# Performance work log

Measured on AMD Instinct MI355X. Metric: run time of the kernel, lower is better.

The kernel has to match this reference:

```python
import jax, jax.numpy as jnp
import numpy as np

N = 50000      # nodes
E = 400000     # edges
F_NODE = 16    # node_features
F_EDGE = 8     # edge_features
H = 16         # hidden_dim
HID_MLP = 32   # edge-MLP hidden width (from MLP([edge_features, 32, ...]))
G = 64         # graphs in batch
T = 2          # num_targets
EPS = 1e-5


def setup_inputs() -> dict:
    key = jax.random.key(0)
    ks = jax.random.split(key, 16)
    def nrm(k, shape, s=0.05):
        return jax.random.normal(k, shape, jnp.float32) * s
    z = lambda *s: jnp.zeros(s, jnp.float32)
    o = lambda *s: jnp.ones(s, jnp.float32)
    inp = {}
    inp['x'] = jax.random.normal(ks[0], (N, F_NODE), jnp.float32)
    inp['edge_attr'] = jax.random.normal(ks[1], (E, F_EDGE), jnp.float32)
    # conv1 edge-MLP: Linear(F_EDGE,32) -> BN -> ReLU -> Linear(32, F_NODE*H)
    inp['e1_W1'] = nrm(ks[2], (F_EDGE, HID_MLP)); inp['e1_b1'] = z(HID_MLP)
    inp['e1_g'] = o(HID_MLP); inp['e1_be'] = z(HID_MLP)
    inp['e1_W2'] = nrm(ks[3], (HID_MLP, F_NODE * H)); inp['e1_b2'] = z(F_NODE * H)
    inp['c1_root'] = nrm(ks[4], (F_NODE, H)); inp['c1_bias'] = z(H)
    # conv2 edge-MLP: Linear(F_EDGE,32) -> BN -> ReLU -> Linear(32, H*H)
    inp['e2_W1'] = nrm(ks[5], (F_EDGE, HID_MLP)); inp['e2_b1'] = z(HID_MLP)
    inp['e2_g'] = o(HID_MLP); inp['e2_be'] = z(HID_MLP)
    inp['e2_W2'] = nrm(ks[6], (HID_MLP, H * H)); inp['e2_b2'] = z(H * H)
    inp['c2_root'] = nrm(ks[7], (H, H)); inp['c2_bias'] = z(H)
    # node batch norms
    inp['bn1_g'] = o(H); inp['bn1_b'] = z(H)
    inp['bn2_g'] = o(H); inp['bn2_b'] = z(H)
    # head MLP
    inp['fc1_W'] = nrm(ks[8], (H, H)); inp['fc1_b'] = z(H)
    inp['fc2_W'] = nrm(ks[9], (H, T)); inp['fc2_b'] = z(T)
    # int args
    inp['edge_index'] = jax.random.randint(ks[10], (2, E), 0, N, dtype=jnp.int32).astype(jnp.int64)
    inp['batch'] = jnp.sort(jax.random.randint(ks[11], (N,), 0, G, dtype=jnp.int32)).astype(jnp.int64)
    return inp


def _bn(h, g, b):
    # training-mode BatchNorm1d: batch stats, biased variance
    m = h.mean(0)
    v = jnp.mean((h - m) ** 2, axis=0)
    return g * (h - m) / jnp.sqrt(v + EPS) + b


def _edge_mlp(e, W1, b1, g, be, W2, b2):
    h = jax.nn.relu(_bn(e @ W1 + b1, g, be))
    return h @ W2 + b2


def _seg_mean(vals, idx, num):
    s = jax.ops.segment_sum(vals, idx, num_segments=num)
    c = jax.ops.segment_sum(jnp.ones((idx.shape[0],), vals.dtype), idx, num_segments=num)
    return s / jnp.maximum(c, 1.0)[:, None]


def _nnconv(x, src, dst, e, W1, b1, g, be, W2, b2, Wroot, bias, in_c, out_c):
    w = _edge_mlp(e, W1, b1, g, be, W2, b2).reshape(-1, in_c, out_c)  # [E, in, out]
    msg = jnp.einsum('ei,eio->eo', x[src], w)                        # gather + per-edge matmul
    agg = _seg_mean(msg, dst, x.shape[0])                            # scatter-mean into targets
    return agg + x @ Wroot + bias


def reference(x, edge_attr, e1_W1, e1_b1, e1_g, e1_be, e1_W2, e1_b2, c1_root, c1_bias,
              e2_W1, e2_b1, e2_g, e2_be, e2_W2, e2_b2, c2_root, c2_bias,
              bn1_g, bn1_b, bn2_g, bn2_b, fc1_W, fc1_b, fc2_W, fc2_b,
              edge_index, batch):
    src, dst = edge_index[0], edge_index[1]
    h = _nnconv(x, src, dst, edge_attr, e1_W1, e1_b1, e1_g, e1_be, e1_W2, e1_b2,
                c1_root, c1_bias, F_NODE, H)
    h = jax.nn.relu(_bn(h, bn1_g, bn1_b))
    h = _nnconv(h, src, dst, edge_attr, e2_W1, e2_b1, e2_g, e2_be, e2_W2, e2_b2,
                c2_root, c2_bias, H, H)
    h = jax.nn.relu(_bn(h, bn2_g, bn2_b))
    pooled = _seg_mean(h, batch, G)          # global_mean_pool -> [G, H]
    out = jax.nn.relu(pooled @ fc1_W + fc1_b) @ fc2_W + fc2_b
    return out
```

## Files before the change

kernel.cpp:

```cpp
#include <hip/hip_runtime.h>

#define N_NODES 50000
#define N_EDGES 400000
#define NG 64
#define NT 2
#define EPS 1e-5f
#define NB_N ((N_NODES + 255) / 256)
#define NB_E ((N_EDGES + 255) / 256)
#define NB_A ((N_NODES + 31) / 32)

constexpr int mom_i(int t) {
    int tt = t - 8; int i = 0;
    while (tt >= 8 - i) { tt -= 8 - i; ++i; }
    return i;
}
constexpr int mom_j(int t) {
    int tt = t - 8; int i = 0;
    while (tt >= 8 - i) { tt -= 8 - i; ++i; }
    return i + tt;
}

template<int IDX>
__device__ __forceinline__ float mom_term(const float* v) {
    if constexpr (IDX >= 44) return 0.f;
    else if constexpr (IDX < 8) return v[IDX];
    else return v[mom_i(IDX)] * v[mom_j(IDX)];
}

template<int BASE>
__device__ __forceinline__ void mom_add16(const float* v, float* acc) {
    acc[0]  += mom_term<BASE + 0>(v);
    acc[1]  += mom_term<BASE + 1>(v);
    acc[2]  += mom_term<BASE + 2>(v);
    acc[3]  += mom_term<BASE + 3>(v);
    acc[4]  += mom_term<BASE + 4>(v);
    acc[5]  += mom_term<BASE + 5>(v);
    acc[6]  += mom_term<BASE + 6>(v);
    acc[7]  += mom_term<BASE + 7>(v);
    acc[8]  += mom_term<BASE + 8>(v);
    acc[9]  += mom_term<BASE + 9>(v);
    acc[10] += mom_term<BASE + 10>(v);
    acc[11] += mom_term<BASE + 11>(v);
    acc[12] += mom_term<BASE + 12>(v);
    acc[13] += mom_term<BASE + 13>(v);
    acc[14] += mom_term<BASE + 14>(v);
    acc[15] += mom_term<BASE + 15>(v);
}

template<int BASE>
__device__ __forceinline__ void mom_loop(
    const float* __restrict__ ea, const int* __restrict__ dst,
    int* __restrict__ deg, float* acc)
{
    const int stride = gridDim.x * 256;
    for (int e = blockIdx.x * 256 + threadIdx.x; e < N_EDGES; e += stride) {
        const float4 a4 = ((const float4*)ea)[e * 2];
        const float4 b4 = ((const float4*)ea)[e * 2 + 1];
        const float v[8] = {a4.x,a4.y,a4.z,a4.w, b4.x,b4.y,b4.z,b4.w};
        if constexpr (BASE == 0) atomicAdd(deg + dst[e], 1);
        mom_add16<BASE>(v, acc);
    }
}

__global__ __launch_bounds__(256) void k_moments(
    const float* __restrict__ ea, const int* __restrict__ dst,
    float* __restrict__ mom, int* __restrict__ deg)
{
    const int c = blockIdx.y;
    float acc[16];
    #pragma unroll
    for (int u = 0; u < 16; ++u) acc[u] = 0.f;
    switch (c) {
        case 0: mom_loop<0 >(ea, dst, deg, acc); break;
        case 1: mom_loop<16>(ea, dst, deg, acc); break;
        default: mom_loop<32>(ea, dst, deg, acc); break;
    }
    __shared__ float red[4][16];
    const int lane = threadIdx.x & 63, wv = threadIdx.x >> 6;
    #pragma unroll
    for (int u = 0; u < 16; ++u) {
        float s = acc[u];
        #pragma unroll
        for (int o = 32; o; o >>= 1) s += __shfl_down(s, o);
        if (lane == 0) red[wv][u] = s;
    }
    __syncthreads();
    if (threadIdx.x < 16) {
        const int idx = c * 16 + threadIdx.x;
        if (idx < 44) {
            const float s = red[0][threadIdx.x] + red[1][threadIdx.x]
                          + red[2][threadIdx.x] + red[3][threadIdx.x];
            atomicAdd(mom + idx, s);
        }
    }
}

__global__ __launch_bounds__(256) void k_scan1(
    const int* __restrict__ deg, int* __restrict__ loc, int* __restrict__ bsum,
    int* __restrict__ hist)
{
    __shared__ int s[256];
    __shared__ int shist[128];
    const int t = threadIdx.x;
    const int n = blockIdx.x * 256 + t;
    const int v = (n < N_NODES) ? deg[n] : 0;
    if (t < 128) shist[t] = 0;
    s[t] = v;
    __syncthreads();
    #pragma unroll
    for (int d = 1; d < 256; d <<= 1) {
        const int a = (t >= d) ? s[t - d] : 0;
        __syncthreads();
        s[t] += a;
        __syncthreads();
    }
    if (n < N_NODES) {
        loc[n] = s[t] - v;
        atomicAdd(&shist[min(v, 127)], 1);
    }
    if (t == 255) bsum[blockIdx.x] = s[t];
    __syncthreads();
    if (t < 128 && shist[t]) atomicAdd(hist + t, shist[t]);
}

__global__ __launch_bounds__(256) void k_singles(
    int* __restrict__ bsum, const float* __restrict__ mom,
    const float* __restrict__ W1a, const float* __restrict__ b1a,
    const float* __restrict__ ga,  const float* __restrict__ bea,
    const float* __restrict__ W1b, const float* __restrict__ b1b,
    const float* __restrict__ gb,  const float* __restrict__ beb,
    float* __restrict__ ss, const int* __restrict__ batch,
    int* __restrict__ start, const int* __restrict__ hist,
    int* __restrict__ cursor)
{
    __shared__ int s[256];
    const int t = threadIdx.x;
    const int v = (t < NB_N) ? bsum[t] : 0;
    s[t] = v;
    __syncthreads();
    #pragma unroll
    for (int d = 1; d < 256; d <<= 1) {
        const int a = (t >= d) ? s[t - d] : 0;
        __syncthreads();
        s[t] += a;
        __syncthreads();
    }
    if (t < NB_N) bsum[t] = s[t] - v;

    if (t < 64) {
        const int m = t >> 5, k = t & 31;
        const float* W1 = m ? W1b : W1a;
        const float b   = (m ? b1b : b1a)[k];
        const float g   = (m ? gb  : ga)[k];
        const float be  = (m ? beb : bea)[k];
        float w[8];
        #pragma unroll
        for (int j = 0; j < 8; ++j) w[j] = W1[j * 32 + k];
        float Sw = 0.f;
        #pragma unroll
        for (int j = 0; j < 8; ++j) Sw += mom[j] * w[j];
        float q = 0.f;
        int idx = 8;
        #pragma unroll
        for (int i = 0; i < 8; ++i)
            #pragma unroll
            for (int j = i; j < 8; ++j) {
                const float Mv = mom[idx++];
                q += Mv * w[i] * w[j] * (i == j ? 1.f : 2.f);
            }
        const float invE  = 1.0f / (float)N_EDGES;
        const float sump  = Sw + (float)N_EDGES * b;
        const float sumpp = q + 2.f * b * Sw + (float)N_EDGES * b * b;
        const float mean  = sump * invE;
        const float var   = fmaxf(sumpp * invE - mean * mean, 0.f);
        const float sc    = g * rsqrtf(var + EPS);
        ss[m * 64 + k]      = sc;
        ss[m * 64 + 32 + k] = be - mean * sc;
    }
    if (t <= NG) {
        int lo = 0, hi = N_NODES;
        while (lo < hi) {
            const int mid = (lo + hi) >> 1;
            if (batch[mid] < t) lo = mid + 1; else hi = mid;
        }
        start[t] = lo;
    }
    if (t == 0) {
        int acc = 0;
        for (int d = 127; d >= 0; --d) { cursor[d] = acc; acc += hist[d]; }
    }
}

__global__ __launch_bounds__(256) void k_scan3(
    const int* __restrict__ loc, const int* __restrict__ bsum,
    const int* __restrict__ deg, int* __restrict__ off, int* __restrict__ cur,
    int* __restrict__ cursor, int* __restrict__ perm)
{
    __shared__ int scnt[128];
    __shared__ int sbase[128];
    const int t = threadIdx.x;
    const int n = blockIdx.x * 256 + t;
    if (t < 128) scnt[t] = 0;
    __syncthreads();
    int b = 0, rk = 0;
    if (n < N_NODES) {
        const int o = loc[n] + bsum[n >> 8];
        off[n] = o; cur[n] = o;
        if (n == 0) off[N_NODES] = N_EDGES;
        b  = min(deg[n], 127);
        rk = atomicAdd(&scnt[b], 1);
    }
    __syncthreads();
    if (t < 128 && scnt[t]) sbase[t] = atomicAdd(cursor + t, scnt[t]);
    __syncthreads();
    if (n < N_NODES) perm[sbase[b] + rk] = n;
}

__global__ __launch_bounds__(256) void k_pos(
    const int* __restrict__ src, const int* __restrict__ dst,
    const float* __restrict__ ea, int* __restrict__ cur,
    int* __restrict__ src_s, float4* __restrict__ ea_s)
{
    const int e = blockIdx.x * 256 + threadIdx.x;
    if (e < N_EDGES) {
        const float4 a4 = ((const float4*)ea)[e * 2];
        const float4 b4 = ((const float4*)ea)[e * 2 + 1];
        const int p = atomicAdd(cur + dst[e], 1);
        src_s[p] = src[e];
        ea_s[p * 2]     = a4;
        ea_s[p * 2 + 1] = b4;
    }
}

__global__ __launch_bounds__(256) void k_agg(
    const float* __restrict__ x, const float4* __restrict__ ea_s,
    const int* __restrict__ src_s, const int* __restrict__ off,
    const int* __restrict__ perm,
    const float* __restrict__ W1, const float* __restrict__ W2,
    const float* __restrict__ ss,
    float* __restrict__ agg_out, float* __restrict__ xsum_out)
{
    __shared__ float4 sW2q[2048];
    const int tid = threadIdx.x;
    #pragma unroll
    for (int i = 0; i < 8; ++i) {
        const int f = tid + 256 * i;
        sW2q[f ^ ((f >> 8) & 7)] = ((const float4*)W2)[f];
    }
    __syncthreads();

    const int c  = tid & 7;
    const int g  = blockIdx.x * 32 + (tid >> 3);
    if (g >= N_NODES) return;
    const int n  = perm[g];

    float w1r[32];
    #pragma unroll
    for (int j = 0; j < 8; ++j)
        #pragma unroll
        for (int kk = 0; kk < 4; ++kk)
            w1r[j * 4 + kk] = W1[j * 32 + c * 4 + kk];
    float scr[4], shr[4];
    #pragma unroll
    for (int kk = 0; kk < 4; ++kk) {
        scr[kk] = ss[c * 4 + kk];
        shr[kk] = ss[32 + c * 4 + kk];
    }

    const int o0 = off[n], o1 = off[n + 1];
    const int len = o1 - o0;
    float T[64];
    #pragma unroll
    for (int j = 0; j < 64; ++j) T[j] = 0.f;
    float xs0 = 0.f, xs1 = 0.f;

    float4 ca, cb, cx0, cx1, cx2, cx3;
    float4 pa, pb;
    int    snn = 0;
    if (len > 0) {
        const int s0 = src_s[o0];
        ca = ea_s[(size_t)o0 * 2];
        cb = ea_s[(size_t)o0 * 2 + 1];
        const float4* xp = (const float4*)(x + (size_t)s0 * 16);
        cx0 = xp[0]; cx1 = xp[1]; cx2 = xp[2]; cx3 = xp[3];
        pa = ca; pb = cb;
        if (len > 1) {
            snn = src_s[o0 + 1];
            pa = ea_s[(size_t)(o0 + 1) * 2];
            pb = ea_s[(size_t)(o0 + 1) * 2 + 1];
        }
    }
    for (int r = 0; r < len; ++r) {
        float4 nx0 = cx0, nx1 = cx1, nx2 = cx2, nx3 = cx3;
        float4 qa = pa, qb = pb;
        int sn2 = snn;
        if (r + 1 < len) {
            const float4* xp = (const float4*)(x + (size_t)snn * 16);
            nx0 = xp[0]; nx1 = xp[1]; nx2 = xp[2]; nx3 = xp[3];
        }
        if (r + 2 < len) {
            sn2 = src_s[o0 + r + 2];
            qa = ea_s[(size_t)(o0 + r + 2) * 2];
            qb = ea_s[(size_t)(o0 + r + 2) * 2 + 1];
        }
        const float ein[8] = {ca.x,ca.y,ca.z,ca.w, cb.x,cb.y,cb.z,cb.w};
        float h[4];
        #pragma unroll
        for (int kk = 0; kk < 4; ++kk) {
            float p = 0.f;
            #pragma unroll
            for (int j = 0; j < 8; ++j) p += ein[j] * w1r[j * 4 + kk];
            h[kk] = fmaxf(p * scr[kk] + shr[kk], 0.f);
        }
        const float xv[16] = {cx0.x,cx0.y,cx0.z,cx0.w, cx1.x,cx1.y,cx1.z,cx1.w,
                              cx2.x,cx2.y,cx2.z,cx2.w, cx3.x,cx3.y,cx3.z,cx3.w};
        #pragma unroll
        for (int kk = 0; kk < 4; ++kk) {
            const float hk = h[kk];
            #pragma unroll
            for (int i = 0; i < 16; ++i) T[kk * 16 + i] += hk * xv[i];
        }
        xs0 += xv[c * 2];
        xs1 += xv[c * 2 + 1];
        ca = pa; cb = pb;
        cx0 = nx0; cx1 = nx1; cx2 = nx2; cx3 = nx3;
        pa = qa; pb = qb; snn = sn2;
    }

    float agg[16];
    #pragma unroll
    for (int o = 0; o < 16; ++o) agg[o] = 0.f;
    #pragma unroll
    for (int kk = 0; kk < 4; ++kk) {
        const int fbase = (c * 4 + kk) * 64;
        #pragma unroll
        for (int i = 0; i < 16; ++i) {
            const float tv = T[kk * 16 + i];
            const int f0 = fbase + i * 4;
            const float4 w0 = sW2q[(f0 + 0) ^ c];
            const float4 w1 = sW2q[(f0 + 1) ^ c];
            const float4 w2 = sW2q[(f0 + 2) ^ c];
            const float4 w3 = sW2q[(f0 + 3) ^ c];
            agg[0]+=tv*w0.x; agg[1]+=tv*w0.y; agg[2]+=tv*w0.z; agg[3]+=tv*w0.w;
            agg[4]+=tv*w1.x; agg[5]+=tv*w1.y; agg[6]+=tv*w1.z; agg[7]+=tv*w1.w;
            agg[8]+=tv*w2.x; agg[9]+=tv*w2.y; agg[10]+=tv*w2.z; agg[11]+=tv*w2.w;
            agg[12]+=tv*w3.x; agg[13]+=tv*w3.y; agg[14]+=tv*w3.z; agg[15]+=tv*w3.w;
        }
    }
    #pragma unroll
    for (int m = 1; m < 8; m <<= 1) {
        #pragma unroll
        for (int o = 0; o < 16; ++o) agg[o] += __shfl_xor(agg[o], m);
    }
    ((float2*)(agg_out  + (size_t)n * 16))[c] = make_float2(agg[c * 2], agg[c * 2 + 1]);
    ((float2*)(xsum_out + (size_t)n * 16))[c] = make_float2(xs0, xs1);
}

__global__ __launch_bounds__(256) void k_node_pre(
    const float* __restrict__ agg, const float* __restrict__ xsum,
    const int* __restrict__ off, const float* __restrict__ xin,
    const float* __restrict__ root, const float* __restrict__ b2,
    const float* __restrict__ bias, float* __restrict__ bnstats,
    float* __restrict__ pre_out)
{
    __shared__ float sroot[256], sb2[256], sbias[16], lacc[32];
    const int tid = threadIdx.x;
    if (tid < 64) {
        ((float4*)sroot)[tid] = ((const float4*)root)[tid];
        ((float4*)sb2)[tid]   = ((const float4*)b2)[tid];
    }
    if (tid < 16) sbias[tid] = bias[tid];
    if (tid < 32) lacc[tid] = 0.f;
    __syncthreads();

    const int n = blockIdx.x * 256 + tid;
    const bool valid = (n < N_NODES);
    float pre[16];
    if (valid) {
        float acc[16];
        const float4* ap = (const float4*)(agg + (size_t)n * 16);
        const float4 a0 = ap[0], a1 = ap[1], a2 = ap[2], a3 = ap[3];
        acc[0]=a0.x; acc[1]=a0.y; acc[2]=a0.z; acc[3]=a0.w;
        acc[4]=a1.x; acc[5]=a1.y; acc[6]=a1.z; acc[7]=a1.w;
        acc[8]=a2.x; acc[9]=a2.y; acc[10]=a2.z; acc[11]=a2.w;
        acc[12]=a3.x; acc[13]=a3.y; acc[14]=a3.z; acc[15]=a3.w;
        const float4* sp = (const float4*)(xsum + (size_t)n * 16);
        const float4 s0 = sp[0], s1 = sp[1], s2 = sp[2], s3 = sp[3];
        const float sv[16] = {s0.x,s0.y,s0.z,s0.w, s1.x,s1.y,s1.z,s1.w,
                              s2.x,s2.y,s2.z,s2.w, s3.x,s3.y,s3.z,s3.w};
        #pragma unroll
        for (int i = 0; i < 16; ++i) {
            const float si = sv[i];
            #pragma unroll
            for (int o = 0; o < 16; ++o) acc[o] += si * sb2[i * 16 + o];
        }
        const float inv = 1.0f / (float)max(off[n + 1] - off[n], 1);
        const float4* xp = (const float4*)(xin + (size_t)n * 16);
        const float4 x0=xp[0],x1=xp[1],x2=xp[2],x3=xp[3];
        const float xn[16] = {x0.x,x0.y,x0.z,x0.w, x1.x,x1.y,x1.z,x1.w,
                              x2.x,x2.y,x2.z,x2.w, x3.x,x3.y,x3.z,x3.w};
        #pragma unroll
        for (int o = 0; o < 16; ++o) pre[o] = sbias[o] + acc[o] * inv;
        #pragma unroll
        for (int i = 0; i < 16; ++i) {
            const float xi = xn[i];
            #pragma unroll
            for (int o = 0; o < 16; ++o) pre[o] += xi * sroot[i * 16 + o];
        }
        float4* wp4 = (float4*)(pre_out + (size_t)n * 16);
        wp4[0] = make_float4(pre[0],pre[1],pre[2],pre[3]);
        wp4[1] = make_float4(pre[4],pre[5],pre[6],pre[7]);
        wp4[2] = make_float4(pre[8],pre[9],pre[10],pre[11]);
        wp4[3] = make_float4(pre[12],pre[13],pre[14],pre[15]);
    } else {
        #pragma unroll
        for (int o = 0; o < 16; ++o) pre[o] = 0.f;
    }
    const int lane = tid & 63;
    #pragma unroll
    for (int o = 0; o < 16; ++o) {
        float s = pre[o], q = s * s;
        #pragma unroll
        for (int w = 32; w; w >>= 1) {
            s += __shfl_down(s, w);
            q += __shfl_down(q, w);
        }
        if (lane == 0) { atomicAdd(&lacc[o], s); atomicAdd(&lacc[16 + o], q); }
    }
    __syncthreads();
    if (tid < 32) atomicAdd(bnstats + tid, lacc[tid]);
}

__global__ __launch_bounds__(256) void k_node_bn(
    const float* __restrict__ pre, const float* __restrict__ bnstats,
    const float* __restrict__ gam, const float* __restrict__ bet,
    float* __restrict__ hout)
{
    __shared__ float sscale[16], sshift[16];
    const int tid = threadIdx.x;
    if (tid < 16) {
        const float mean = bnstats[tid] * (1.0f / N_NODES);
        const float var  = fmaxf(bnstats[16 + tid] * (1.0f / N_NODES) - mean * mean, 0.f);
        const float rs   = rsqrtf(var + EPS);
        const float sc   = gam[tid] * rs;
        sscale[tid] = sc;
        sshift[tid] = bet[tid] - mean * sc;
    }
    __syncthreads();
    const int n = blockIdx.x * 256 + tid;
    if (n >= N_NODES) return;
    const float4* pp = (const float4*)(pre + (size_t)n * 16);
    const float4 p0=pp[0],p1=pp[1],p2=pp[2],p3=pp[3];
    const float pv[16] = {p0.x,p0.y,p0.z,p0.w, p1.x,p1.y,p1.z,p1.w,
                          p2.x,p2.y,p2.z,p2.w, p3.x,p3.y,p3.z,p3.w};
    float h[16];
    #pragma unroll
    for (int o = 0; o < 16; ++o) h[o] = fmaxf(pv[o] * sscale[o] + sshift[o], 0.f);
    float4* hp = (float4*)(hout + (size_t)n * 16);
    hp[0] = make_float4(h[0],h[1],h[2],h[3]);
    hp[1] = make_float4(h[4],h[5],h[6],h[7]);
    hp[2] = make_float4(h[8],h[9],h[10],h[11]);
    hp[3] = make_float4(h[12],h[13],h[14],h[15]);
}

__global__ __launch_bounds__(256) void k_pool_bn(
    const float* __restrict__ pre, const float* __restrict__ bnstats,
    const float* __restrict__ gam, const float* __restrict__ bet,
    const int* __restrict__ start, float* __restrict__ pool)
{
    __shared__ float lds[16][16];
    __shared__ float sscale[16], sshift[16];
    const int tid = threadIdx.x;
    if (tid < 16) {
        const float mean = bnstats[tid] * (1.0f / N_NODES);
        const float var  = fmaxf(bnstats[16 + tid] * (1.0f / N_NODES) - mean * mean, 0.f);
        const float rs   = rsqrtf(var + EPS);
        const float sc   = gam[tid] * rs;
        sscale[tid] = sc;
        sshift[tid] = bet[tid] - mean * sc;
    }
    __syncthreads();
    const int g = blockIdx.x;
    const int c = tid & 15, rg = tid >> 4;
    const int s = start[g], e = start[g + 1];
    const float sc = sscale[c], sh = sshift[c];
    float acc = 0.f;
    for (int r = s + rg; r < e; r += 16)
        acc += fmaxf(pre[(size_t)r * 16 + c] * sc + sh, 0.f);
    lds[rg][c] = acc;
    __syncthreads();
    if (tid < 16) {
        float sum = 0.f;
        #pragma unroll
        for (int i = 0; i < 16; ++i) sum += lds[i][tid];
        const float inv = 1.0f / (float)max(e - s, 1);
        pool[g * 16 + tid] = sum * inv;
    }
}

__global__ __launch_bounds__(64) void k_head(
    const float* __restrict__ pool,
    const float* __restrict__ fc1W, const float* __restrict__ fc1b,
    const float* __restrict__ fc2W, const float* __restrict__ fc2b,
    float* __restrict__ out)
{
    const int g = threadIdx.x;
    if (g >= NG) return;
    float p[16];
    #pragma unroll
    for (int o = 0; o < 16; ++o) p[o] = pool[g * 16 + o];
    float z[16];
    #pragma unroll
    for (int j = 0; j < 16; ++j) {
        float a = fc1b[j];
        #pragma unroll
        for (int o = 0; o < 16; ++o) a += p[o] * fc1W[o * 16 + j];
        z[j] = fmaxf(a, 0.f);
    }
    #pragma unroll
    for (int t = 0; t < NT; ++t) {
        float a = fc2b[t];
        #pragma unroll
        for (int j = 0; j < 16; ++j) a += z[j] * fc2W[j * 2 + t];
        out[g * 2 + t] = a;
    }
}

extern "C" void kernel_launch(void* const* d_in, const int* in_sizes, int n_in,
                              void* d_out, int out_size, void* d_ws, size_t ws_size,
                              hipStream_t stream)
{
    const float* x    = (const float*)d_in[0];
    const float* ea   = (const float*)d_in[1];
    const float* e1W1 = (const float*)d_in[2];  const float* e1b1 = (const float*)d_in[3];
    const float* e1g  = (const float*)d_in[4];  const float* e1be = (const float*)d_in[5];
    const float* e1W2 = (const float*)d_in[6];  const float* e1b2 = (const float*)d_in[7];
    const float* c1r  = (const float*)d_in[8];  const float* c1b  = (const float*)d_in[9];
    const float* e2W1 = (const float*)d_in[10]; const float* e2b1 = (const float*)d_in[11];
    const float* e2g  = (const float*)d_in[12]; const float* e2be = (const float*)d_in[13];
    const float* e2W2 = (const float*)d_in[14]; const float* e2b2 = (const float*)d_in[15];
    const float* c2r  = (const float*)d_in[16]; const float* c2b  = (const float*)d_in[17];
    const float* bn1g = (const float*)d_in[18]; const float* bn1b = (const float*)d_in[19];
    const float* bn2g = (const float*)d_in[20]; const float* bn2b = (const float*)d_in[21];
    const float* fc1W = (const float*)d_in[22]; const float* fc1b = (const float*)d_in[23];
    const float* fc2W = (const float*)d_in[24]; const float* fc2b = (const float*)d_in[25];
    const int* eidx   = (const int*)d_in[26];
    const int* batch  = (const int*)d_in[27];
    const int* src = eidx;
    const int* dst = eidx + N_EDGES;

    float* ws      = (float*)d_ws;
    float* mom     = ws;
    float* bnstats = ws + 64;
    float* ss      = ws + 128;
    int* hist_i    = (int*)(ws + 256);
    int* cursor_i  = (int*)(ws + 384);
    int* deg_i   = (int*)(ws + 512);
    int* loc_i   = deg_i + N_NODES;
    int* cur_i   = loc_i + N_NODES;
    int* bsum_i  = cur_i + N_NODES;
    int* start_i = bsum_i + 256;
    int* off_i   = start_i + 72;
    int* perm_i  = off_i + N_NODES + 8;
    int* src_s   = perm_i + N_NODES;
    const size_t fo = 512 + 256 + 72 + 8 + 5 * (size_t)N_NODES + (size_t)N_EDGES;
    float* ea_s  = ws + fo;
    float* aggb  = ea_s + (size_t)N_EDGES * 8;
    float* xsumb = aggb + (size_t)N_NODES * 16;
    float* pre1  = xsumb + (size_t)N_NODES * 16;
    float* h1n   = pre1 + (size_t)N_NODES * 16;
    float* pool  = h1n + (size_t)N_NODES * 16;

    hipMemsetAsync(d_ws, 0, (size_t)(512 + N_NODES) * sizeof(float), stream);

    k_moments<<<dim3(512, 3), 256, 0, stream>>>(ea, dst, mom, deg_i);
    k_scan1<<<NB_N, 256, 0, stream>>>(deg_i, loc_i, bsum_i, hist_i);
    k_singles<<<1, 256, 0, stream>>>(bsum_i, mom, e1W1, e1b1, e1g, e1be,
                                     e2W1, e2b1, e2g, e2be, ss, batch, start_i,
                                     hist_i, cursor_i);
    k_scan3<<<NB_N, 256, 0, stream>>>(loc_i, bsum_i, deg_i, off_i, cur_i,
                                      cursor_i, perm_i);
    k_pos<<<NB_E, 256, 0, stream>>>(src, dst, ea, cur_i, src_s, (float4*)ea_s);

    k_agg<<<NB_A, 256, 0, stream>>>(x, (const float4*)ea_s, src_s, off_i, perm_i,
                                    e1W1, e1W2, ss, aggb, xsumb);
    k_node_pre<<<NB_N, 256, 0, stream>>>(aggb, xsumb, off_i, x, c1r, e1b2,
                                         c1b, bnstats, pre1);
    k_node_bn<<<NB_N, 256, 0, stream>>>(pre1, bnstats, bn1g, bn1b, h1n);

    k_agg<<<NB_A, 256, 0, stream>>>(h1n, (const float4*)ea_s, src_s, off_i, perm_i,
                                    e2W1, e2W2, ss + 64, aggb, xsumb);
    k_node_pre<<<NB_N, 256, 0, stream>>>(aggb, xsumb, off_i, h1n, c2r, e2b2,
                                         c2b, bnstats + 32, pre1);

    k_pool_bn<<<NG, 256, 0, stream>>>(pre1, bnstats + 32, bn2g, bn2b, start_i, pool);
    k_head<<<1, 64, 0, stream>>>(pool, fc1W, fc1b, fc2W, fc2b, (float*)d_out);
}
```

Baseline: 237.0 us.

## Fuse moment passes into one sweep and simplify k_agg prefetch and projection indexing

k_moments now computes all 44 edge-attribute moments in a single pass over the edges with 48 accumulators per thread on a 1-D grid of 192 blocks. Previously it ran three grid slices that each re-read edge_attr. In k_agg the prefetch loop drops its bounds checks: src_s and ea_s are padded with a few dummy entries so reads past the segment stay safe. The per-thread xsum values now come from a direct float2 load, the loop is unrolled by two, and the W2 projection uses precomputed base pointers with a simpler XOR swizzle. The changes are meant to cut redundant global reads and branch and index overhead, at the cost of more registers, possibly lower occupancy, and workspace layout shifts that must stay consistent.

```diff
diff --git a/kernel.cpp b/kernel.cpp
--- a/kernel.cpp
+++ b/kernel.cpp
@@ -47,51 +47,37 @@
     acc[15] += mom_term<BASE + 15>(v);
 }
 
-template<int BASE>
-__device__ __forceinline__ void mom_loop(
+__global__ __launch_bounds__(256) void k_moments(
     const float* __restrict__ ea, const int* __restrict__ dst,
-    int* __restrict__ deg, float* acc)
-{
+    float* __restrict__ mom, int* __restrict__ deg)
+{
+    float acc[48];
+    #pragma unroll
+    for (int u = 0; u < 48; ++u) acc[u] = 0.f;
     const int stride = gridDim.x * 256;
     for (int e = blockIdx.x * 256 + threadIdx.x; e < N_EDGES; e += stride) {
         const float4 a4 = ((const float4*)ea)[e * 2];
         const float4 b4 = ((const float4*)ea)[e * 2 + 1];
         const float v[8] = {a4.x,a4.y,a4.z,a4.w, b4.x,b4.y,b4.z,b4.w};
-        if constexpr (BASE == 0) atomicAdd(deg + dst[e], 1);
-        mom_add16<BASE>(v, acc);
-    }
-}
-
-__global__ __launch_bounds__(256) void k_moments(
-    const float* __restrict__ ea, const int* __restrict__ dst,
-    float* __restrict__ mom, int* __restrict__ deg)
-{
-    const int c = blockIdx.y;
-    float acc[16];
-    #pragma unroll
-    for (int u = 0; u < 16; ++u) acc[u] = 0.f;
-    switch (c) {
-        case 0: mom_loop<0 >(ea, dst, deg, acc); break;
-        case 1: mom_loop<16>(ea, dst, deg, acc); break;
-        default: mom_loop<32>(ea, dst, deg, acc); break;
-    }
-    __shared__ float red[4][16];
+        atomicAdd(deg + dst[e], 1);
+        mom_add16<0 >(v, acc);
+        mom_add16<16>(v, acc + 16);
+        mom_add16<32>(v, acc + 32);
+    }
+    __shared__ float red[4][48];
     const int lane = threadIdx.x & 63, wv = threadIdx.x >> 6;
     #pragma unroll
-    for (int u = 0; u < 16; ++u) {
+    for (int u = 0; u < 48; ++u) {
         float s = acc[u];
         #pragma unroll
         for (int o = 32; o; o >>= 1) s += __shfl_down(s, o);
         if (lane == 0) red[wv][u] = s;
     }
     __syncthreads();
-    if (threadIdx.x < 16) {
-        const int idx = c * 16 + threadIdx.x;
-        if (idx < 44) {
-            const float s = red[0][threadIdx.x] + red[1][threadIdx.x]
-                          + red[2][threadIdx.x] + red[3][threadIdx.x];
-            atomicAdd(mom + idx, s);
-        }
+    if (threadIdx.x < 44) {
+        const float s = red[0][threadIdx.x] + red[1][threadIdx.x]
+                      + red[2][threadIdx.x] + red[3][threadIdx.x];
+        atomicAdd(mom + threadIdx.x, s);
     }
 }
 
@@ -229,8 +215,27 @@
         src_s[p] = src[e];
         ea_s[p * 2]     = a4;
         ea_s[p * 2 + 1] = b4;
-    }
-}
+        if (e < 4) src_s[N_EDGES + e] = 0;
+    }
+}
+
+#define PROJ(IX)                                                              \
+    _Pragma("unroll")                                                         \
+    for (int kk = 0; kk < 4; ++kk) {                                          \
+        _Pragma("unroll")                                                     \
+        for (int i = 0; i < 16; ++i) {                                        \
+            const float tv = T[kk * 16 + i];                                  \
+            const int fo4 = kk * 64 + ((i ^ IX) << 2);                        \
+            const float4 w0 = pk0[fo4];                                       \
+            const float4 w1 = pk1[fo4];                                       \
+            const float4 w2 = pk2[fo4];                                       \
+            const float4 w3 = pk3[fo4];                                       \
+            agg[0]+=tv*w0.x; agg[1]+=tv*w0.y; agg[2]+=tv*w0.z; agg[3]+=tv*w0.w;\
+            agg[4]+=tv*w1.x; agg[5]+=tv*w1.y; agg[6]+=tv*w1.z; agg[7]+=tv*w1.w;\
+            agg[8]+=tv*w2.x; agg[9]+=tv*w2.y; agg[10]+=tv*w2.z; agg[11]+=tv*w2.w;\
+            agg[12]+=tv*w3.x; agg[13]+=tv*w3.y; agg[14]+=tv*w3.z; agg[15]+=tv*w3.w;\
+        }                                                                     \
+    }
 
 __global__ __launch_bounds__(256) void k_agg(
     const float* __restrict__ x, const float4* __restrict__ ea_s,
@@ -274,35 +279,32 @@
     for (int j = 0; j < 64; ++j) T[j] = 0.f;
     float xs0 = 0.f, xs1 = 0.f;
 
-    float4 ca, cb, cx0, cx1, cx2, cx3;
-    float4 pa, pb;
+    float4 ca = make_float4(0,0,0,0), cb = ca;
+    float4 cx0 = ca, cx1 = ca, cx2 = ca, cx3 = ca;
+    float2 cxs = make_float2(0, 0);
+    float4 pa = ca, pb = ca;
     int    snn = 0;
+    const int* sp2 = src_s + o0 + 2;
+    const float4* ep2 = ea_s + (size_t)(o0 + 2) * 2;
     if (len > 0) {
         const int s0 = src_s[o0];
         ca = ea_s[(size_t)o0 * 2];
         cb = ea_s[(size_t)o0 * 2 + 1];
-        const float4* xp = (const float4*)(x + (size_t)s0 * 16);
+        const float4* xp = (const float4*)(x + (s0 << 4));
         cx0 = xp[0]; cx1 = xp[1]; cx2 = xp[2]; cx3 = xp[3];
-        pa = ca; pb = cb;
-        if (len > 1) {
-            snn = src_s[o0 + 1];
-            pa = ea_s[(size_t)(o0 + 1) * 2];
-            pb = ea_s[(size_t)(o0 + 1) * 2 + 1];
-        }
-    }
+        cxs = *(const float2*)(x + (s0 << 4) + (c << 1));
+        snn = src_s[o0 + 1];
+        pa = ea_s[(size_t)(o0 + 1) * 2];
+        pb = ea_s[(size_t)(o0 + 1) * 2 + 1];
+    }
+    #pragma unroll 2
     for (int r = 0; r < len; ++r) {
-        float4 nx0 = cx0, nx1 = cx1, nx2 = cx2, nx3 = cx3;
-        float4 qa = pa, qb = pb;
-        int sn2 = snn;
-        if (r + 1 < len) {
-            const float4* xp = (const float4*)(x + (size_t)snn * 16);
-            nx0 = xp[0]; nx1 = xp[1]; nx2 = xp[2]; nx3 = xp[3];
-        }
-        if (r + 2 < len) {
-            sn2 = src_s[o0 + r + 2];
-            qa = ea_s[(size_t)(o0 + r + 2) * 2];
-            qb = ea_s[(size_t)(o0 + r + 2) * 2 + 1];
-        }
+        const float4* xp = (const float4*)(x + (snn << 4));
+        const float4 nx0 = xp[0], nx1 = xp[1], nx2 = xp[2], nx3 = xp[3];
+        const float2 nxs = *(const float2*)(x + (snn << 4) + (c << 1));
+        const int sn2 = sp2[r];
+        const float4 qa = ep2[(size_t)r * 2];
+        const float4 qb = ep2[(size_t)r * 2 + 1];
         const float ein[8] = {ca.x,ca.y,ca.z,ca.w, cb.x,cb.y,cb.z,cb.w};
         float h[4];
         #pragma unroll
@@ -320,33 +322,24 @@
             #pragma unroll
             for (int i = 0; i < 16; ++i) T[kk * 16 + i] += hk * xv[i];
         }
-        xs0 += xv[c * 2];
-        xs1 += xv[c * 2 + 1];
-        ca = pa; cb = pb;
+        xs0 += cxs.x;
+        xs1 += cxs.y;
+        ca = pa; cb = pb; pa = qa; pb = qb;
         cx0 = nx0; cx1 = nx1; cx2 = nx2; cx3 = nx3;
-        pa = qa; pb = qb; snn = sn2;
-    }
-
+        cxs = nxs; snn = sn2;
+    }
+
+    const int cA = c & 3;
+    const int iX = (c >> 2) & 1;
+    const float4* pk0 = sW2q + (c << 8) + (0 ^ cA);
+    const float4* pk1 = sW2q + (c << 8) + (1 ^ cA);
+    const float4* pk2 = sW2q + (c << 8) + (2 ^ cA);
+    const float4* pk3 = sW2q + (c << 8) + (3 ^ cA);
     float agg[16];
     #pragma unroll
     for (int o = 0; o < 16; ++o) agg[o] = 0.f;
-    #pragma unroll
-    for (int kk = 0; kk < 4; ++kk) {
-        const int fbase = (c * 4 + kk) * 64;
-        #pragma unroll
-        for (int i = 0; i < 16; ++i) {
-            const float tv = T[kk * 16 + i];
-            const int f0 = fbase + i * 4;
-            const float4 w0 = sW2q[(f0 + 0) ^ c];
-            const float4 w1 = sW2q[(f0 + 1) ^ c];
-            const float4 w2 = sW2q[(f0 + 2) ^ c];
-            const float4 w3 = sW2q[(f0 + 3) ^ c];
-            agg[0]+=tv*w0.x; agg[1]+=tv*w0.y; agg[2]+=tv*w0.z; agg[3]+=tv*w0.w;
-            agg[4]+=tv*w1.x; agg[5]+=tv*w1.y; agg[6]+=tv*w1.z; agg[7]+=tv*w1.w;
-            agg[8]+=tv*w2.x; agg[9]+=tv*w2.y; agg[10]+=tv*w2.z; agg[11]+=tv*w2.w;
-            agg[12]+=tv*w3.x; agg[13]+=tv*w3.y; agg[14]+=tv*w3.z; agg[15]+=tv*w3.w;
-        }
-    }
+    if (iX == 0) { PROJ(0) } else { PROJ(1) }
+
     #pragma unroll
     for (int m = 1; m < 8; m <<= 1) {
         #pragma unroll
@@ -563,9 +556,9 @@
     int* off_i   = start_i + 72;
     int* perm_i  = off_i + N_NODES + 8;
     int* src_s   = perm_i + N_NODES;
-    const size_t fo = 512 + 256 + 72 + 8 + 5 * (size_t)N_NODES + (size_t)N_EDGES;
+    const size_t fo = 512 + 256 + 72 + 8 + 5 * (size_t)N_NODES + (size_t)N_EDGES + 8;
     float* ea_s  = ws + fo;
-    float* aggb  = ea_s + (size_t)N_EDGES * 8;
+    float* aggb  = ea_s + (size_t)(N_EDGES + 4) * 8;
     float* xsumb = aggb + (size_t)N_NODES * 16;
     float* pre1  = xsumb + (size_t)N_NODES * 16;
     float* h1n   = pre1 + (size_t)N_NODES * 16;
@@ -573,7 +566,7 @@
 
     hipMemsetAsync(d_ws, 0, (size_t)(512 + N_NODES) * sizeof(float), stream);
 
-    k_moments<<<dim3(512, 3), 256, 0, stream>>>(ea, dst, mom, deg_i);
+    k_moments<<<192, 256, 0, stream>>>(ea, dst, mom, deg_i);
     k_scan1<<<NB_N, 256, 0, stream>>>(deg_i, loc_i, bsum_i, hist_i);
     k_singles<<<1, 256, 0, stream>>>(bsum_i, mom, e1W1, e1b1, e1g, e1be,
                                      e2W1, e2b1, e2g, e2be, ss, batch, start_i,
```

Measured after the change: 411.1 us. +73.5%, slower.

## Fuse node pre-activation and BN partial stats into aggregation kernel

Applied to the files above, without the earlier changes.

The separate k_node_pre pass is folded into k_agg. Each 8-thread group now applies the b2/xsum term, mean normalisation, root projection and bias directly, and writes per-block BN sum and sum-of-squares partials instead of doing global atomics. The downstream BN kernels reduce those partials themselves, so the agg/xsum intermediate buffers and two kernel launches go away. The cost is redundant partial reduction in every BN block and extra LDS and register pressure in k_agg.

```diff
diff --git a/kernel.cpp b/kernel.cpp
--- a/kernel.cpp
+++ b/kernel.cpp
@@ -8,6 +8,7 @@
 #define NB_N ((N_NODES + 255) / 256)
 #define NB_E ((N_EDGES + 255) / 256)
 #define NB_A ((N_NODES + 31) / 32)
+#define PCHUNK ((NB_A + 7) / 8)
 
 constexpr int mom_i(int t) {
     int tt = t - 8; int i = 0;
@@ -237,22 +238,30 @@
     const int* __restrict__ src_s, const int* __restrict__ off,
     const int* __restrict__ perm,
     const float* __restrict__ W1, const float* __restrict__ W2,
-    const float* __restrict__ ss,
-    float* __restrict__ agg_out, float* __restrict__ xsum_out)
+    const float* __restrict__ ss, const float* __restrict__ root,
+    const float* __restrict__ b2, const float* __restrict__ bias,
+    float* __restrict__ pre_out, float* __restrict__ partials)
 {
     __shared__ float4 sW2q[2048];
+    __shared__ float sroot[256], sb2[256], sbias[16], lacc[32];
     const int tid = threadIdx.x;
     #pragma unroll
     for (int i = 0; i < 8; ++i) {
         const int f = tid + 256 * i;
         sW2q[f ^ ((f >> 8) & 7)] = ((const float4*)W2)[f];
     }
+    if (tid < 64) {
+        ((float4*)sroot)[tid] = ((const float4*)root)[tid];
+        ((float4*)sb2)[tid]   = ((const float4*)b2)[tid];
+    }
+    if (tid < 16) sbias[tid] = bias[tid];
+    if (tid < 32) lacc[tid] = 0.f;
     __syncthreads();
 
     const int c  = tid & 7;
     const int g  = blockIdx.x * 32 + (tid >> 3);
-    if (g >= N_NODES) return;
-    const int n  = perm[g];
+    const bool valid = (g < N_NODES);
+    const int n  = perm[valid ? g : (N_NODES - 1)];
 
     float w1r[32];
     #pragma unroll
@@ -274,8 +283,10 @@
     for (int j = 0; j < 64; ++j) T[j] = 0.f;
     float xs0 = 0.f, xs1 = 0.f;
 
-    float4 ca, cb, cx0, cx1, cx2, cx3;
-    float4 pa, pb;
+    float4 ca = make_float4(0,0,0,0), cb = ca;
+    float4 cx0 = ca, cx1 = ca, cx2 = ca, cx3 = ca;
+    float2 cxs = make_float2(0.f, 0.f);
+    float4 pa = ca, pb = ca;
     int    snn = 0;
     if (len > 0) {
         const int s0 = src_s[o0];
@@ -283,6 +294,7 @@
         cb = ea_s[(size_t)o0 * 2 + 1];
         const float4* xp = (const float4*)(x + (size_t)s0 * 16);
         cx0 = xp[0]; cx1 = xp[1]; cx2 = xp[2]; cx3 = xp[3];
+        cxs = *(const float2*)(x + (size_t)s0 * 16 + (c << 1));
         pa = ca; pb = cb;
         if (len > 1) {
             snn = src_s[o0 + 1];
@@ -292,11 +304,13 @@
     }
     for (int r = 0; r < len; ++r) {
         float4 nx0 = cx0, nx1 = cx1, nx2 = cx2, nx3 = cx3;
+        float2 nxs = cxs;
         float4 qa = pa, qb = pb;
         int sn2 = snn;
         if (r + 1 < len) {
             const float4* xp = (const float4*)(x + (size_t)snn * 16);
             nx0 = xp[0]; nx1 = xp[1]; nx2 = xp[2]; nx3 = xp[3];
+            nxs = *(const float2*)(x + (size_t)snn * 16 + (c << 1));
         }
         if (r + 2 < len) {
             sn2 = src_s[o0 + r + 2];
@@ -320,10 +334,11 @@
             #pragma unroll
             for (int i = 0; i < 16; ++i) T[kk * 16 + i] += hk * xv[i];
         }
-        xs0 += xv[c * 2];
-        xs1 += xv[c * 2 + 1];
+        xs0 += cxs.x;
+        xs1 += cxs.y;
         ca = pa; cb = pb;
         cx0 = nx0; cx1 = nx1; cx2 = nx2; cx3 = nx3;
+        cxs = nxs;
         pa = qa; pb = qb; snn = sn2;
     }
 
@@ -352,101 +367,89 @@
         #pragma unroll
         for (int o = 0; o < 16; ++o) agg[o] += __shfl_xor(agg[o], m);
     }
-    ((float2*)(agg_out  + (size_t)n * 16))[c] = make_float2(agg[c * 2], agg[c * 2 + 1]);
-    ((float2*)(xsum_out + (size_t)n * 16))[c] = make_float2(xs0, xs1);
-}
-
-__global__ __launch_bounds__(256) void k_node_pre(
-    const float* __restrict__ agg, const float* __restrict__ xsum,
-    const int* __restrict__ off, const float* __restrict__ xin,
-    const float* __restrict__ root, const float* __restrict__ b2,
-    const float* __restrict__ bias, float* __restrict__ bnstats,
-    float* __restrict__ pre_out)
-{
-    __shared__ float sroot[256], sb2[256], sbias[16], lacc[32];
+
+    const int gb = (tid & 63) & 56;
+    float xsum[16];
+    #pragma unroll
+    for (int i = 0; i < 8; ++i) {
+        xsum[2 * i]     = __shfl(xs0, gb + i);
+        xsum[2 * i + 1] = __shfl(xs1, gb + i);
+    }
+    const int c0 = c * 2, c1 = c * 2 + 1;
+    float p0 = agg[c * 2], p1 = agg[c * 2 + 1];
+    #pragma unroll
+    for (int i = 0; i < 16; ++i) {
+        p0 += xsum[i] * sb2[i * 16 + c0];
+        p1 += xsum[i] * sb2[i * 16 + c1];
+    }
+    const float invd = 1.0f / (float)max(len, 1);
+    p0 = p0 * invd + sbias[c0];
+    p1 = p1 * invd + sbias[c1];
+    const float4* xrp = (const float4*)(x + (size_t)n * 16);
+    const float4 r0 = xrp[0], r1 = xrp[1], r2 = xrp[2], r3 = xrp[3];
+    const float xn[16] = {r0.x,r0.y,r0.z,r0.w, r1.x,r1.y,r1.z,r1.w,
+                          r2.x,r2.y,r2.z,r2.w, r3.x,r3.y,r3.z,r3.w};
+    #pragma unroll
+    for (int i = 0; i < 16; ++i) {
+        p0 += xn[i] * sroot[i * 16 + c0];
+        p1 += xn[i] * sroot[i * 16 + c1];
+    }
+    if (valid) {
+        ((float2*)(pre_out + (size_t)n * 16))[c] = make_float2(p0, p1);
+    } else { p0 = 0.f; p1 = 0.f; }
+    float q0 = p0 * p0, q1 = p1 * p1;
+    #pragma unroll
+    for (int m = 8; m < 64; m <<= 1) {
+        p0 += __shfl_xor(p0, m); p1 += __shfl_xor(p1, m);
+        q0 += __shfl_xor(q0, m); q1 += __shfl_xor(q1, m);
+    }
+    if ((tid & 63) < 8) {
+        atomicAdd(&lacc[c0], p0);       atomicAdd(&lacc[c1], p1);
+        atomicAdd(&lacc[16 + c0], q0);  atomicAdd(&lacc[16 + c1], q1);
+    }
+    __syncthreads();
+    if (tid < 32) partials[(size_t)tid * NB_A + blockIdx.x] = lacc[tid];
+}
+
+__device__ __forceinline__ void bn_from_partials(
+    const float* __restrict__ partials, const float* __restrict__ gam,
+    const float* __restrict__ bet, float* sscale, float* sshift, float* red)
+{
     const int tid = threadIdx.x;
-    if (tid < 64) {
-        ((float4*)sroot)[tid] = ((const float4*)root)[tid];
-        ((float4*)sb2)[tid]   = ((const float4*)b2)[tid];
-    }
-    if (tid < 16) sbias[tid] = bias[tid];
-    if (tid < 32) lacc[tid] = 0.f;
-    __syncthreads();
-
-    const int n = blockIdx.x * 256 + tid;
-    const bool valid = (n < N_NODES);
-    float pre[16];
-    if (valid) {
-        float acc[16];
-        const float4* ap = (const float4*)(agg + (size_t)n * 16);
-        const float4 a0 = ap[0], a1 = ap[1], a2 = ap[2], a3 = ap[3];
-        acc[0]=a0.x; acc[1]=a0.y; acc[2]=a0.z; acc[3]=a0.w;
-        acc[4]=a1.x; acc[5]=a1.y; acc[6]=a1.z; acc[7]=a1.w;
-        acc[8]=a2.x; acc[9]=a2.y; acc[10]=a2.z; acc[11]=a2.w;
-        acc[12]=a3.x; acc[13]=a3.y; acc[14]=a3.z; acc[15]=a3.w;
-        const float4* sp = (const float4*)(xsum + (size_t)n * 16);
-        const float4 s0 = sp[0], s1 = sp[1], s2 = sp[2], s3 = sp[3];
-        const float sv[16] = {s0.x,s0.y,s0.z,s0.w, s1.x,s1.y,s1.z,s1.w,
-                              s2.x,s2.y,s2.z,s2.w, s3.x,s3.y,s3.z,s3.w};
-        #pragma unroll
-        for (int i = 0; i < 16; ++i) {
-            const float si = sv[i];
-            #pragma unroll
-            for (int o = 0; o < 16; ++o) acc[o] += si * sb2[i * 16 + o];
-        }
-        const float inv = 1.0f / (float)max(off[n + 1] - off[n], 1);
-        const float4* xp = (const float4*)(xin + (size_t)n * 16);
-        const float4 x0=xp[0],x1=xp[1],x2=xp[2],x3=xp[3];
-        const float xn[16] = {x0.x,x0.y,x0.z,x0.w, x1.x,x1.y,x1.z,x1.w,
-                              x2.x,x2.y,x2.z,x2.w, x3.x,x3.y,x3.z,x3.w};
-        #pragma unroll
-        for (int o = 0; o < 16; ++o) pre[o] = sbias[o] + acc[o] * inv;
-        #pragma unroll
-        for (int i = 0; i < 16; ++i) {
-            const float xi = xn[i];
-            #pragma unroll
-            for (int o = 0; o < 16; ++o) pre[o] += xi * sroot[i * 16 + o];
-        }
-        float4* wp4 = (float4*)(pre_out + (size_t)n * 16);
-        wp4[0] = make_float4(pre[0],pre[1],pre[2],pre[3]);
-        wp4[1] = make_float4(pre[4],pre[5],pre[6],pre[7]);
-        wp4[2] = make_float4(pre[8],pre[9],pre[10],pre[11]);
-        wp4[3] = make_float4(pre[12],pre[13],pre[14],pre[15]);
-    } else {
-        #pragma unroll
-        for (int o = 0; o < 16; ++o) pre[o] = 0.f;
-    }
-    const int lane = tid & 63;
-    #pragma unroll
-    for (int o = 0; o < 16; ++o) {
-        float s = pre[o], q = s * s;
-        #pragma unroll
-        for (int w = 32; w; w >>= 1) {
-            s += __shfl_down(s, w);
-            q += __shfl_down(q, w);
-        }
-        if (lane == 0) { atomicAdd(&lacc[o], s); atomicAdd(&lacc[16 + o], q); }
-    }
-    __syncthreads();
-    if (tid < 32) atomicAdd(bnstats + tid, lacc[tid]);
-}
-
-__global__ __launch_bounds__(256) void k_node_bn(
-    const float* __restrict__ pre, const float* __restrict__ bnstats,
-    const float* __restrict__ gam, const float* __restrict__ bet,
-    float* __restrict__ hout)
-{
-    __shared__ float sscale[16], sshift[16];
-    const int tid = threadIdx.x;
+    const int ch = tid & 31, sg = tid >> 5;
+    const int beg = sg * PCHUNK;
+    const int end = min(beg + PCHUNK, NB_A);
+    float s = 0.f;
+    for (int i = beg; i < end; ++i) s += partials[(size_t)ch * NB_A + i];
+    red[ch * 8 + sg] = s;
+    __syncthreads();
+    if (tid < 32) {
+        float t = 0.f;
+        #pragma unroll
+        for (int i = 0; i < 8; ++i) t += red[tid * 8 + i];
+        red[256 + tid] = t;
+    }
+    __syncthreads();
     if (tid < 16) {
-        const float mean = bnstats[tid] * (1.0f / N_NODES);
-        const float var  = fmaxf(bnstats[16 + tid] * (1.0f / N_NODES) - mean * mean, 0.f);
+        const float mean = red[256 + tid] * (1.0f / N_NODES);
+        const float var  = fmaxf(red[256 + 16 + tid] * (1.0f / N_NODES) - mean * mean, 0.f);
         const float rs   = rsqrtf(var + EPS);
         const float sc   = gam[tid] * rs;
         sscale[tid] = sc;
         sshift[tid] = bet[tid] - mean * sc;
     }
     __syncthreads();
+}
+
+__global__ __launch_bounds__(256) void k_node_bn(
+    const float* __restrict__ pre, const float* __restrict__ partials,
+    const float* __restrict__ gam, const float* __restrict__ bet,
+    float* __restrict__ hout)
+{
+    __shared__ float sscale[16], sshift[16];
+    __shared__ float red[288];
+    bn_from_partials(partials, gam, bet, sscale, sshift, red);
+    const int tid = threadIdx.x;
     const int n = blockIdx.x * 256 + tid;
     if (n >= N_NODES) return;
     const float4* pp = (const float4*)(pre + (size_t)n * 16);
@@ -464,22 +467,15 @@
 }
 
 __global__ __launch_bounds__(256) void k_pool_bn(
-    const float* __restrict__ pre, const float* __restrict__ bnstats,
+    const float* __restrict__ pre, const float* __restrict__ partials,
     const float* __restrict__ gam, const float* __restrict__ bet,
     const int* __restrict__ start, float* __restrict__ pool)
 {
+    __shared__ float sscale[16], sshift[16];
+    __shared__ float red[288];
     __shared__ float lds[16][16];
-    __shared__ float sscale[16], sshift[16];
+    bn_from_partials(partials, gam, bet, sscale, sshift, red);
     const int tid = threadIdx.x;
-    if (tid < 16) {
-        const float mean = bnstats[tid] * (1.0f / N_NODES);
-        const float var  = fmaxf(bnstats[16 + tid] * (1.0f / N_NODES) - mean * mean, 0.f);
-        const float rs   = rsqrtf(var + EPS);
-        const float sc   = gam[tid] * rs;
-        sscale[tid] = sc;
-        sshift[tid] = bet[tid] - mean * sc;
-    }
-    __syncthreads();
     const int g = blockIdx.x;
     const int c = tid & 15, rg = tid >> 4;
     const int s = start[g], e = start[g + 1];
@@ -551,11 +547,10 @@
 
     float* ws      = (float*)d_ws;
     float* mom     = ws;
-    float* bnstats = ws + 64;
-    float* ss      = ws + 128;
-    int* hist_i    = (int*)(ws + 256);
-    int* cursor_i  = (int*)(ws + 384);
-    int* deg_i   = (int*)(ws + 512);
+    float* ss      = ws + 64;
+    int* hist_i    = (int*)(ws + 192);
+    int* cursor_i  = (int*)(ws + 320);
+    int* deg_i   = (int*)(ws + 448);
     int* loc_i   = deg_i + N_NODES;
     int* cur_i   = loc_i + N_NODES;
     int* bsum_i  = cur_i + N_NODES;
@@ -563,15 +558,15 @@
     int* off_i   = start_i + 72;
     int* perm_i  = off_i + N_NODES + 8;
     int* src_s   = perm_i + N_NODES;
-    const size_t fo = 512 + 256 + 72 + 8 + 5 * (size_t)N_NODES + (size_t)N_EDGES;
+    const size_t fo = 448 + 256 + 72 + 8 + 5 * (size_t)N_NODES + (size_t)N_EDGES;
     float* ea_s  = ws + fo;
-    float* aggb  = ea_s + (size_t)N_EDGES * 8;
-    float* xsumb = aggb + (size_t)N_NODES * 16;
-    float* pre1  = xsumb + (size_t)N_NODES * 16;
+    float* part1 = ea_s + (size_t)N_EDGES * 8;
+    float* part2 = part1 + 32 * (size_t)NB_A;
+    float* pre1  = part2 + 32 * (size_t)NB_A;
     float* h1n   = pre1 + (size_t)N_NODES * 16;
     float* pool  = h1n + (size_t)N_NODES * 16;
 
-    hipMemsetAsync(d_ws, 0, (size_t)(512 + N_NODES) * sizeof(float), stream);
+    hipMemsetAsync(d_ws, 0, (size_t)(448 + N_NODES) * sizeof(float), stream);
 
     k_moments<<<dim3(512, 3), 256, 0, stream>>>(ea, dst, mom, deg_i);
     k_scan1<<<NB_N, 256, 0, stream>>>(deg_i, loc_i, bsum_i, hist_i);
@@ -583,16 +578,11 @@
     k_pos<<<NB_E, 256, 0, stream>>>(src, dst, ea, cur_i, src_s, (float4*)ea_s);
 
     k_agg<<<NB_A, 256, 0, stream>>>(x, (const float4*)ea_s, src_s, off_i, perm_i,
-                                    e1W1, e1W2, ss, aggb, xsumb);
-    k_node_pre<<<NB_N, 256, 0, stream>>>(aggb, xsumb, off_i, x, c1r, e1b2,
-                                         c1b, bnstats, pre1);
-    k_node_bn<<<NB_N, 256, 0, stream>>>(pre1, bnstats, bn1g, bn1b, h1n);
+                                    e1W1, e1W2, ss, c1r, e1b2, c1b, pre1, part1);
+    k_node_bn<<<NB_N, 256, 0, stream>>>(pre1, part1, bn1g, bn1b, h1n);
 
     k_agg<<<NB_A, 256, 0, stream>>>(h1n, (const float4*)ea_s, src_s, off_i, perm_i,
-                                    e2W1, e2W2, ss + 64, aggb, xsumb);
-    k_node_pre<<<NB_N, 256, 0, stream>>>(aggb, xsumb, off_i, h1n, c2r, e2b2,
-                                         c2b, bnstats + 32, pre1);
-
-    k_pool_bn<<<NG, 256, 0, stream>>>(pre1, bnstats + 32, bn2g, bn2b, start_i, pool);
+                                    e2W1, e2W2, ss + 64, c2r, e2b2, c2b, pre1, part2);
+    k_pool_bn<<<NG, 256, 0, stream>>>(pre1, part2, bn2g, bn2b, start_i, pool);
     k_head<<<1, 64, 0, stream>>>(pool, fc1W, fc1b, fc2W, fc2b, (float*)d_out);
 }
```

After: 321.2 us. +35.5%, slower.
